# Kernel optimization log

Measured on AMD Instinct MI355X. Metric: run time of the kernel, lower is better.

Reference implementation:

```python
import jax, jax.numpy as jnp
import numpy as np

N = 100000   # nodes
E = 1600000  # edges (avg degree 16)
IN, HID, OUT = 128, 128, 64
EPS = 1e-5


def setup_inputs() -> dict:
    key = jax.random.key(0)
    ks = jax.random.split(key, 8)
    x = jax.random.normal(ks[0], (N, IN), dtype=jnp.float32)
    edge_index = jax.random.randint(ks[1], (2, E), 0, N, dtype=jnp.int64)

    def w(k, i, o):
        return jax.random.normal(k, (i, o), dtype=jnp.float32) / np.float32(np.sqrt(i))

    return {
        'x': x,
        'edge_index': edge_index,
        'W1': w(ks[2], IN, HID), 'b1': jnp.zeros((HID,), jnp.float32),
        'g1': jnp.ones((HID,), jnp.float32), 'be1': jnp.zeros((HID,), jnp.float32),
        'W2': w(ks[3], HID, HID), 'b2': jnp.zeros((HID,), jnp.float32),
        'g2': jnp.ones((HID,), jnp.float32), 'be2': jnp.zeros((HID,), jnp.float32),
        'W3': w(ks[4], HID, OUT), 'b3': jnp.zeros((OUT,), jnp.float32),
    }


def gcn_conv(x, W, b, src, dst, n):
    # GCNConv: x' = D^{-1/2} (A + I) D^{-1/2} X W + b
    h = x @ W                                   # [N, F_out]
    loop = jnp.arange(n, dtype=src.dtype)
    s = jnp.concatenate([src, loop])            # self-loops appended
    d = jnp.concatenate([dst, loop])
    deg = jax.ops.segment_sum(jnp.ones_like(d, dtype=h.dtype), d, num_segments=n)
    dinv = jax.lax.rsqrt(jnp.maximum(deg, 1.0))  # deg >= 1 due to self-loops
    norm = dinv[s] * dinv[d]                     # [E+N]
    out = jax.ops.segment_sum(h[s] * norm[:, None], d, num_segments=n)
    return out + b


def batch_norm(x, gamma, beta):
    m = x.mean(axis=0)
    v = x.var(axis=0)  # biased variance, as used for normalization in torch BN
    return (x - m) * jax.lax.rsqrt(v + EPS) * gamma + beta


def reference(x, edge_index, W1, b1, g1, be1, W2, b2, g2, be2, W3, b3):
    src, dst = edge_index[0], edge_index[1]
    r = x                                        # residual (skip = Identity, in_dim == hidden_dim)
    h = batch_norm(gcn_conv(x, W1, b1, src, dst, N), g1, be1) + r
    r = h
    h = jax.nn.relu(h)                           # dropout p=0 -> identity
    h = batch_norm(gcn_conv(h, W2, b2, src, dst, N), g2, be2) + r
    h = jax.nn.relu(h)
    out = gcn_conv(h, W3, b3, src, dst, N)       # last layer: no bn/skip/relu
    return out
```

## Files before the change

kernel.cpp:

```cpp
#include <hip/hip_runtime.h>

static constexpr int kN = 100000;
static constexpr int kE = 1600000;
static constexpr float kEps = 1e-5f;

static constexpr int kBSH = 9;
static constexpr int kNB = (kN + 511) >> kBSH;
static constexpr int kBCAP = 12288;
static constexpr int kCHUNK = 4096;
static constexpr int kPad = 16;

typedef __attribute__((ext_vector_type(8))) short short8;
typedef __attribute__((ext_vector_type(4))) float float4v;
typedef __attribute__((ext_vector_type(2))) float float2v;

static __device__ inline unsigned short f2bf(float f) {
  union { float f; unsigned int u; } v; v.f = f;
  unsigned int r = v.u + 0x7fffu + ((v.u >> 16) & 1u);
  return (unsigned short)(r >> 16);
}
static __device__ inline float bf2f(unsigned int bits16) {
  union { unsigned int u; float f; } v; v.u = bits16 << 16; return v.f;
}
static __device__ inline unsigned int pack2bf(float lo, float hi) {
  return (unsigned int)f2bf(lo) | ((unsigned int)f2bf(hi) << 16);
}

__global__ __launch_bounds__(512) void bin_k(const int* __restrict__ src,
                                             const int* __restrict__ dst,
                                             int* __restrict__ gcursor,
                                             int2* __restrict__ gstage) {
  __shared__ int s_cnt[256];
  __shared__ int s_scan[256];
  __shared__ int s_base[256];
  __shared__ int s_cur[256];
  __shared__ int s_gb[256];
  __shared__ int2 s_stage[kCHUNK];
  int tid = threadIdx.x;
  int e0 = blockIdx.x * kCHUNK;
  int n = kE - e0; if (n > kCHUNK) n = kCHUNK;
  if (tid < 256) s_cnt[tid] = 0;
  __syncthreads();
  for (int j = tid; j < n; j += 512) {
    atomicAdd(&s_cnt[dst[e0 + j] >> kBSH], 1);
  }
  __syncthreads();
  int v = 0;
  if (tid < 256) { v = s_cnt[tid]; s_scan[tid] = v; }
  __syncthreads();
  #pragma unroll
  for (int o = 1; o < 256; o <<= 1) {
    int t = (tid >= o && tid < 256) ? s_scan[tid - o] : 0;
    __syncthreads();
    if (tid < 256) s_scan[tid] += t;
    __syncthreads();
  }
  if (tid < 256) {
    int excl = s_scan[tid] - v;
    s_base[tid] = excl;
    s_cur[tid] = excl;
  }
  __syncthreads();
  if (tid < kNB && s_cnt[tid] > 0) s_gb[tid] = atomicAdd(&gcursor[tid], s_cnt[tid]);
  for (int j = tid; j < n; j += 512) {
    int s = src[e0 + j];
    int d = dst[e0 + j];
    int p = atomicAdd(&s_cur[d >> kBSH], 1);
    s_stage[p] = make_int2(s, d);
  }
  __syncthreads();
  for (int j = tid; j < n; j += 512) {
    int2 e = s_stage[j];
    int b = e.y >> kBSH;
    gstage[(size_t)b * kBCAP + s_gb[b] + (j - s_base[b])] = e;
  }
}

__global__ __launch_bounds__(256) void alloc_hist_k(const int2* __restrict__ gstage,
                                                    const int* __restrict__ gcursor,
                                                    int* __restrict__ counter,
                                                    int* __restrict__ deg,
                                                    int* __restrict__ row_start,
                                                    float* __restrict__ dinv) {
  __shared__ int s_deg[1 << kBSH];
  __shared__ int s_scan[256];
  __shared__ int s_bcast;
  int b = blockIdx.x, tid = threadIdx.x;
  int n0 = b << kBSH;
  s_deg[tid] = 0;
  s_deg[tid + 256] = 0;
  __syncthreads();
  int cnt = gcursor[b];
  const int2* seg = gstage + (size_t)b * kBCAP;
  for (int j = tid; j < cnt; j += 256) {
    atomicAdd(&s_deg[seg[j].y - n0], 1);
  }
  __syncthreads();
  int i0 = 2 * tid, i1 = 2 * tid + 1;
  int d0 = s_deg[i0], d1 = s_deg[i1];
  int pd0 = (d0 + kPad - 1) & ~(kPad - 1);
  int pd1 = (d1 + kPad - 1) & ~(kPad - 1);
  int sum = pd0 + pd1;
  s_scan[tid] = sum;
  __syncthreads();
  #pragma unroll
  for (int o = 1; o < 256; o <<= 1) {
    int t = (tid >= o) ? s_scan[tid - o] : 0;
    __syncthreads();
    s_scan[tid] += t;
    __syncthreads();
  }
  if (tid == 255) s_bcast = atomicAdd(counter, s_scan[255]);
  __syncthreads();
  int base = s_bcast + s_scan[tid] - sum;
  int node0 = n0 + i0, node1 = n0 + i1;
  if (node0 < kN) {
    deg[node0] = d0;
    row_start[node0] = base;
    dinv[node0] = rsqrtf((float)(d0 + 1));
  }
  if (node1 < kN) {
    deg[node1] = d1;
    row_start[node1] = base + pd0;
    dinv[node1] = rsqrtf((float)(d1 + 1));
  }
}

__global__ __launch_bounds__(256) void scatter2_k(const int2* __restrict__ gstage,
                                                  const int* __restrict__ gcursor,
                                                  const int* __restrict__ rowst,
                                                  const int* __restrict__ deg,
                                                  int* __restrict__ csr_src) {
  __shared__ int s_cur[1 << kBSH];
  int b = blockIdx.x, tid = threadIdx.x;
  int n0 = b << kBSH;
  int nn = kN - n0; if (nn > (1 << kBSH)) nn = 1 << kBSH;
  for (int i = tid; i < nn; i += 256) s_cur[i] = rowst[n0 + i];
  __syncthreads();
  int cnt = gcursor[b];
  const int2* seg = gstage + (size_t)b * kBCAP;
  for (int j = tid; j < cnt; j += 256) {
    int2 e = seg[j];
    int pos = atomicAdd(&s_cur[e.y - n0], 1);
    csr_src[pos] = e.x;
  }
  __syncthreads();
  for (int i = tid; i < nn; i += 256) {
    int d = deg[n0 + i];
    int endp = rowst[n0 + i] + ((d + kPad - 1) & ~(kPad - 1));
    for (int p = s_cur[i]; p < endp; ++p) csr_src[p] = kN;
  }
}

__global__ void convert_w_all_k(const float* __restrict__ W1, const float* __restrict__ W2,
                                const float* __restrict__ W3,
                                unsigned short* __restrict__ wf1,
                                unsigned short* __restrict__ wf2,
                                unsigned short* __restrict__ wf3,
                                unsigned char* __restrict__ hF8,
                                unsigned short* __restrict__ hH) {
  int tid = blockIdx.x * blockDim.x + threadIdx.x;
  const float* W;
  unsigned short* Wf;
  int BNO;
  if (tid < 2048) { W = W1; Wf = wf1; BNO = 128; }
  else if (tid < 4096) { W = W2; Wf = wf2; BNO = 128; tid -= 2048; }
  else if (tid < 5120) { W = W3; Wf = wf3; BNO = 64; tid -= 4096; }
  else if (tid < 5152) {
    ((unsigned int*)(hF8 + (size_t)kN * 128))[tid - 5120] = 0u;
    return;
  } else if (tid < 5184) {
    ((unsigned int*)(hH + (size_t)kN * 64))[tid - 5152] = 0u;
    return;
  } else return;
  int l = tid & 63;
  int frag = tid >> 6;
  int q = frag & 3;
  int t = frag >> 2;
  int n = t * 16 + (l & 15);
  int kbase = q * 32 + ((l >> 4) << 3);
  unsigned short v[8] __attribute__((aligned(16)));
  #pragma unroll
  for (int j = 0; j < 8; ++j) v[j] = f2bf(W[(kbase + j) * BNO + n]);
  ((uint4*)Wf)[tid] = *(const uint4*)v;
}

template <int BNO, bool AF32, bool OUT8>
__global__ __launch_bounds__(256) void gemm_mfma_k(const void* __restrict__ Aptr,
                                                   const unsigned short* __restrict__ Wf,
                                                   const float* __restrict__ dinv,
                                                   void* __restrict__ Cptr,
                                                   float* __restrict__ stats) {
  if (stats && blockIdx.x == 0) stats[threadIdx.x] = 0.f;
  int wid = (int)((blockIdx.x * blockDim.x + threadIdx.x) >> 6);
  if (wid >= kN / 16) return;
  int l = threadIdx.x & 63;
  int r0 = wid * 16;
  short8 a[4];
  if constexpr (AF32) {
    const float* Af = (const float*)Aptr + (size_t)(r0 + (l & 15)) * 128 + ((l >> 4) << 3);
    #pragma unroll
    for (int q = 0; q < 4; ++q) {
      float4 u0 = *(const float4*)(Af + q * 32);
      float4 u1 = *(const float4*)(Af + q * 32 + 4);
      short8 t;
      t[0] = (short)f2bf(u0.x); t[1] = (short)f2bf(u0.y);
      t[2] = (short)f2bf(u0.z); t[3] = (short)f2bf(u0.w);
      t[4] = (short)f2bf(u1.x); t[5] = (short)f2bf(u1.y);
      t[6] = (short)f2bf(u1.z); t[7] = (short)f2bf(u1.w);
      a[q] = t;
    }
  } else {
    const short8* Arow =
        (const short8*)((const unsigned short*)Aptr + (size_t)(r0 + (l & 15)) * 128 + ((l >> 4) << 3));
    #pragma unroll
    for (int q = 0; q < 4; ++q) a[q] = Arow[q * 4];
  }
  const short8* Wv = (const short8*)Wf + l;
  constexpr int NT = BNO / 16;
  float4v acc[NT];
  #pragma unroll
  for (int t = 0; t < NT; ++t) {
    acc[t] = (float4v){0.f, 0.f, 0.f, 0.f};
    #pragma unroll
    for (int q = 0; q < 4; ++q) {
      short8 b = Wv[(t * 4 + q) * 64];
      acc[t] = __builtin_amdgcn_mfma_f32_16x16x32_bf16(a[q], b, acc[t], 0, 0, 0);
    }
  }
  int orow = r0 + ((l >> 4) << 2);
  int ocol = l & 15;
  float dv[4];
  #pragma unroll
  for (int r = 0; r < 4; ++r) dv[r] = dinv[orow + r];
  #pragma unroll
  for (int t = 0; t < NT; ++t) {
    #pragma unroll
    for (int r = 0; r < 4; ++r) {
      float val = acc[t][r] * dv[r];
      if constexpr (OUT8) {
        unsigned int u = __builtin_amdgcn_cvt_pk_fp8_f32(val, val, 0u, false);
        ((unsigned char*)Cptr)[(size_t)(orow + r) * BNO + t * 16 + ocol] = (unsigned char)(u & 0xffu);
      } else {
        ((unsigned short*)Cptr)[(size_t)(orow + r) * BNO + t * 16 + ocol] = f2bf(val);
      }
    }
  }
}

__global__ __launch_bounds__(256) void aggregate128_k(
    const unsigned char* __restrict__ H8, const int* __restrict__ row_start,
    const int* __restrict__ deg, const int* __restrict__ csr_src,
    const float* __restrict__ dinv, const float* __restrict__ bias,
    unsigned int* __restrict__ outp, float* __restrict__ stats) {
  __shared__ float s_sum[128], s_sq[128];
  int tid = threadIdx.x;
  if (tid < 128) { s_sum[tid] = 0.f; s_sq[tid] = 0.f; }
  __syncthreads();
  int lane = tid & 63;
  int qt = lane >> 4;
  int ql = lane & 15;
  int nwaves = gridDim.x * (blockDim.x >> 6);
  int gwave = (int)((blockIdx.x * blockDim.x + tid) >> 6);
  const uint2* H2 = (const uint2*)H8;
  float4 blo = ((const float4*)bias)[2 * ql];
  float4 bhi = ((const float4*)bias)[2 * ql + 1];
  float st[8] = {0.f, 0.f, 0.f, 0.f, 0.f, 0.f, 0.f, 0.f};
  float sqa[8] = {0.f, 0.f, 0.f, 0.f, 0.f, 0.f, 0.f, 0.f};
  auto accum = [](float (&a)[8], uint2 v) {
    float2v p0 = __builtin_amdgcn_cvt_pk_f32_fp8(v.x, false);
    float2v p1 = __builtin_amdgcn_cvt_pk_f32_fp8(v.x, true);
    float2v p2 = __builtin_amdgcn_cvt_pk_f32_fp8(v.y, false);
    float2v p3 = __builtin_amdgcn_cvt_pk_f32_fp8(v.y, true);
    a[0] += p0.x; a[1] += p0.y; a[2] += p1.x; a[3] += p1.y;
    a[4] += p2.x; a[5] += p2.y; a[6] += p3.x; a[7] += p3.y;
  };
  int node = gwave;
  int rs = 0, pd = 0;
  float di = 1.f;
  int ec = kN;
  if (node < kN) {
    rs = row_start[node];
    pd = (deg[node] + kPad - 1) & ~(kPad - 1);
    di = dinv[node];
    ec = csr_src[rs + lane];
  }
  while (node < kN) {
    int cur_rs = rs, cur_pd = pd, cur_e = ec;
    float cur_di = di;
    int nxt = node + nwaves;
    if (nxt < kN) {
      rs = row_start[nxt];
      pd = (deg[nxt] + kPad - 1) & ~(kPad - 1);
      di = dinv[nxt];
      ec = csr_src[rs + lane];
    }
    float a[8] = {0.f, 0.f, 0.f, 0.f, 0.f, 0.f, 0.f, 0.f};
    uint2 vself = H2[(size_t)node * 16 + ql];
    int nb = cur_pd >> 4;
    int nb4 = nb > 4 ? 4 : nb;
    for (int i = 0; i < nb4; ++i) {
      int s[4];
      uint2 v[4];
      #pragma unroll
      for (int j = 0; j < 4; ++j) s[j] = __shfl(cur_e, i * 16 + 4 * j + qt, 64);
      #pragma unroll
      for (int j = 0; j < 4; ++j) v[j] = H2[(size_t)s[j] * 16 + ql];
      #pragma unroll
      for (int j = 0; j < 4; ++j) accum(a, v[j]);
    }
    for (int i = 4; i < nb; ++i) {
      int ee = csr_src[cur_rs + i * 16 + (lane & 15)];
      int s[4];
      uint2 v[4];
      #pragma unroll
      for (int j = 0; j < 4; ++j) s[j] = __shfl(ee, 4 * j + qt, 64);
      #pragma unroll
      for (int j = 0; j < 4; ++j) v[j] = H2[(size_t)s[j] * 16 + ql];
      #pragma unroll
      for (int j = 0; j < 4; ++j) accum(a, v[j]);
    }
    #pragma unroll
    for (int j = 0; j < 8; ++j) {
      a[j] += __shfl_xor(a[j], 16, 64);
      a[j] += __shfl_xor(a[j], 32, 64);
    }
    accum(a, vself);
    float o[8];
    o[0] = cur_di * a[0] + blo.x; o[1] = cur_di * a[1] + blo.y;
    o[2] = cur_di * a[2] + blo.z; o[3] = cur_di * a[3] + blo.w;
    o[4] = cur_di * a[4] + bhi.x; o[5] = cur_di * a[5] + bhi.y;
    o[6] = cur_di * a[6] + bhi.z; o[7] = cur_di * a[7] + bhi.w;
    if (qt == 0) {
      uint4 ov;
      ov.x = pack2bf(o[0], o[1]); ov.y = pack2bf(o[2], o[3]);
      ov.z = pack2bf(o[4], o[5]); ov.w = pack2bf(o[6], o[7]);
      ((uint4*)outp)[(size_t)node * 16 + ql] = ov;
      #pragma unroll
      for (int j = 0; j < 8; ++j) { st[j] += o[j]; sqa[j] += o[j] * o[j]; }
    }
    node = nxt;
  }
  if (qt == 0) {
    #pragma unroll
    for (int j = 0; j < 8; ++j) {
      atomicAdd(&s_sum[8 * ql + j], st[j]);
      atomicAdd(&s_sq[8 * ql + j], sqa[j]);
    }
  }
  __syncthreads();
  if (tid < 128) {
    atomicAdd(&stats[tid], s_sum[tid]);
    atomicAdd(&stats[128 + tid], s_sq[tid]);
  }
}

__global__ __launch_bounds__(256) void aggregate64_k(
    const unsigned short* __restrict__ Hb, const int* __restrict__ row_start,
    const int* __restrict__ deg, const int* __restrict__ csr_src,
    const float* __restrict__ dinv, const float* __restrict__ bias,
    float* __restrict__ outp) {
  int tid = threadIdx.x;
  int lane = tid & 63;
  int qt = lane >> 4;
  int ql = lane & 15;
  int nwaves = gridDim.x * (blockDim.x >> 6);
  int gwave = (int)((blockIdx.x * blockDim.x + tid) >> 6);
  const uint2* H2 = (const uint2*)Hb;
  float4 b4 = ((const float4*)bias)[ql];
  auto accum = [](float (&a)[4], uint2 v) {
    a[0] += bf2f(v.x & 0xffffu); a[1] += bf2f(v.x >> 16);
    a[2] += bf2f(v.y & 0xffffu); a[3] += bf2f(v.y >> 16);
  };
  int node = gwave;
  int rs = 0, pd = 0;
  float di = 1.f;
  int ec = kN;
  if (node < kN) {
    rs = row_start[node];
    pd = (deg[node] + kPad - 1) & ~(kPad - 1);
    di = dinv[node];
    ec = csr_src[rs + lane];
  }
  while (node < kN) {
    int cur_rs = rs, cur_pd = pd, cur_e = ec;
    float cur_di = di;
    int nxt = node + nwaves;
    if (nxt < kN) {
      rs = row_start[nxt];
      pd = (deg[nxt] + kPad - 1) & ~(kPad - 1);
      di = dinv[nxt];
      ec = csr_src[rs + lane];
    }
    float a[4] = {0.f, 0.f, 0.f, 0.f};
    uint2 vself = H2[(size_t)node * 16 + ql];
    int nb = cur_pd >> 4;
    int nb4 = nb > 4 ? 4 : nb;
    for (int i = 0; i < nb4; ++i) {
      int s[4];
      uint2 v[4];
      #pragma unroll
      for (int j = 0; j < 4; ++j) s[j] = __shfl(cur_e, i * 16 + 4 * j + qt, 64);
      #pragma unroll
      for (int j = 0; j < 4; ++j) v[j] = H2[(size_t)s[j] * 16 + ql];
      #pragma unroll
      for (int j = 0; j < 4; ++j) accum(a, v[j]);
    }
    for (int i = 4; i < nb; ++i) {
      int ee = csr_src[cur_rs + i * 16 + (lane & 15)];
      int s[4];
      uint2 v[4];
      #pragma unroll
      for (int j = 0; j < 4; ++j) s[j] = __shfl(ee, 4 * j + qt, 64);
      #pragma unroll
      for (int j = 0; j < 4; ++j) v[j] = H2[(size_t)s[j] * 16 + ql];
      #pragma unroll
      for (int j = 0; j < 4; ++j) accum(a, v[j]);
    }
    #pragma unroll
    for (int j = 0; j < 4; ++j) {
      a[j] += __shfl_xor(a[j], 16, 64);
      a[j] += __shfl_xor(a[j], 32, 64);
    }
    accum(a, vself);
    if (qt == 0) {
      ((float4*)outp)[(size_t)node * 16 + ql] =
          make_float4(cur_di * a[0] + b4.x, cur_di * a[1] + b4.y,
                      cur_di * a[2] + b4.z, cur_di * a[3] + b4.w);
    }
    node = nxt;
  }
}

template <bool WRITE_Z, bool RF32>
__global__ void bn_apply_res_k(const unsigned int* __restrict__ a, const void* __restrict__ rp,
                               const float* __restrict__ stats, const float* __restrict__ g,
                               const float* __restrict__ be, unsigned int* __restrict__ z,
                               unsigned int* __restrict__ rb) {
  __shared__ float lss[256];
  int t = threadIdx.x;
  if (t < 128) {
    float mean = stats[t] * (1.f / kN);
    float var = stats[128 + t] * (1.f / kN) - mean * mean;
    float inv = rsqrtf(var + kEps);
    float sc = g[t] * inv;
    lss[t] = sc;
    lss[128 + t] = be[t] - mean * sc;
  }
  __syncthreads();
  int idx = blockIdx.x * blockDim.x + t;
  if (idx >= kN * 16) return;
  uint4 av = ((const uint4*)a)[idx];
  float r[8];
  if constexpr (RF32) {
    float4 r0 = ((const float4*)rp)[idx * 2];
    float4 r1 = ((const float4*)rp)[idx * 2 + 1];
    r[0] = r0.x; r[1] = r0.y; r[2] = r0.z; r[3] = r0.w;
    r[4] = r1.x; r[5] = r1.y; r[6] = r1.z; r[7] = r1.w;
  } else {
    uint4 rv = ((const uint4*)rp)[idx];
    r[0] = bf2f(rv.x & 0xffffu); r[1] = bf2f(rv.x >> 16);
    r[2] = bf2f(rv.y & 0xffffu); r[3] = bf2f(rv.y >> 16);
    r[4] = bf2f(rv.z & 0xffffu); r[5] = bf2f(rv.z >> 16);
    r[6] = bf2f(rv.w & 0xffffu); r[7] = bf2f(rv.w >> 16);
  }
  int c = (idx & 15) * 8;
  float o[8];
  unsigned int apk[4] = {av.x, av.y, av.z, av.w};
  #pragma unroll
  for (int j = 0; j < 4; ++j) {
    o[2 * j]     = lss[c + 2 * j] * bf2f(apk[j] & 0xffffu) + lss[128 + c + 2 * j] + r[2 * j];
    o[2 * j + 1] = lss[c + 2 * j + 1] * bf2f(apk[j] >> 16) + lss[128 + c + 2 * j + 1] + r[2 * j + 1];
  }
  if (WRITE_Z) {
    uint4 zv;
    zv.x = pack2bf(o[0], o[1]); zv.y = pack2bf(o[2], o[3]);
    zv.z = pack2bf(o[4], o[5]); zv.w = pack2bf(o[6], o[7]);
    ((uint4*)z)[idx] = zv;
  }
  uint4 hv;
  hv.x = pack2bf(fmaxf(o[0], 0.f), fmaxf(o[1], 0.f));
  hv.y = pack2bf(fmaxf(o[2], 0.f), fmaxf(o[3], 0.f));
  hv.z = pack2bf(fmaxf(o[4], 0.f), fmaxf(o[5], 0.f));
  hv.w = pack2bf(fmaxf(o[6], 0.f), fmaxf(o[7], 0.f));
  ((uint4*)rb)[idx] = hv;
}

extern "C" void kernel_launch(void* const* d_in, const int* in_sizes, int n_in,
                              void* d_out, int out_size, void* d_ws, size_t ws_size,
                              hipStream_t stream) {
  const float* x   = (const float*)d_in[0];
  const int*   ei  = (const int*)d_in[1];
  const float* W1  = (const float*)d_in[2];
  const float* b1  = (const float*)d_in[3];
  const float* g1  = (const float*)d_in[4];
  const float* be1 = (const float*)d_in[5];
  const float* W2  = (const float*)d_in[6];
  const float* b2  = (const float*)d_in[7];
  const float* g2  = (const float*)d_in[8];
  const float* be2 = (const float*)d_in[9];
  const float* W3  = (const float*)d_in[10];
  const float* b3  = (const float*)d_in[11];
  float* outp = (float*)d_out;

  const int* src = ei;
  const int* dst = ei + kE;

  char* ws = (char*)d_ws;
  size_t off = 0;
  auto alloc = [&](size_t bytes) -> void* {
    void* p = ws + off;
    off = (off + bytes + 255) & ~size_t(255);
    return p;
  };
  unsigned char* hF8 = (unsigned char*)alloc((size_t)(kN + 1) * 128);
  unsigned short* hH = (unsigned short*)alloc((size_t)(kN + 1) * 64 * 2);
  unsigned int* aB = (unsigned int*)alloc((size_t)kN * 64 * 4);
  unsigned int* zC = (unsigned int*)alloc((size_t)kN * 64 * 4);
  unsigned int* hb = (unsigned int*)alloc((size_t)kN * 64 * 4);
  int*   csr_src  = (int*)alloc((size_t)(3200000 + 64) * 4);
  int2*  gstage   = (int2*)alloc((size_t)kNB * kBCAP * 8);
  int*   gcursor  = (int*)alloc((kNB + 1) * 4);
  int*   counter  = gcursor + kNB;
  int*   deg      = (int*)alloc((size_t)kN * 4);
  float* dinv     = (float*)alloc((size_t)kN * 4);
  int*   rowst    = (int*)alloc((size_t)kN * 4);
  float* stats    = (float*)alloc(256 * 4);
  unsigned short* wf1 = (unsigned short*)alloc(128 * 128 * 2);
  unsigned short* wf2 = (unsigned short*)alloc(128 * 128 * 2);
  unsigned short* wf3 = (unsigned short*)alloc(128 * 64 * 2);

  const int TB = 256;
  int blkBin = (kE + kCHUNK - 1) / kCHUNK;
  int blkGemm = (kN / 16 + 3) / 4;
  int blkApply = kN * 16 / TB;
  const int blkAgg = 2048;

  hipMemsetAsync(gcursor, 0, (kNB + 1) * 4, stream);
  bin_k<<<blkBin, 512, 0, stream>>>(src, dst, gcursor, gstage);
  alloc_hist_k<<<kNB, TB, 0, stream>>>(gstage, gcursor, counter, deg, rowst, dinv);
  scatter2_k<<<kNB, TB, 0, stream>>>(gstage, gcursor, rowst, deg, csr_src);
  convert_w_all_k<<<21, TB, 0, stream>>>(W1, W2, W3, wf1, wf2, wf3, hF8, hH);

  gemm_mfma_k<128, true, true><<<blkGemm, 256, 0, stream>>>(x, wf1, dinv, hF8, stats);
  aggregate128_k<<<blkAgg, TB, 0, stream>>>(hF8, rowst, deg, csr_src, dinv, b1, aB, stats);
  bn_apply_res_k<true, true><<<blkApply, TB, 0, stream>>>(aB, x, stats, g1, be1, zC, hb);

  gemm_mfma_k<128, false, true><<<blkGemm, 256, 0, stream>>>((const unsigned short*)hb, wf2, dinv, hF8, stats);
  aggregate128_k<<<blkAgg, TB, 0, stream>>>(hF8, rowst, deg, csr_src, dinv, b2, aB, stats);
  bn_apply_res_k<false, false><<<blkApply, TB, 0, stream>>>(aB, zC, stats, g2, be2, nullptr, hb);

  gemm_mfma_k<64, false, false><<<blkGemm, 256, 0, stream>>>((const unsigned short*)hb, wf3, dinv, hH, nullptr);
  aggregate64_k<<<blkAgg, TB, 0, stream>>>(hH, rowst, deg, csr_src, dinv, b3, outp);
}
```

Baseline: 423.8 us.

## Fuse batch-norm apply and residual into next GEMM prologue, add nontemporal loads

Removes the separate bn_apply_res kernels and folds BN scale/shift, residual add, ReLU and bf16 packing into the A-operand load of the following MFMA GEMM. This drops the intermediate hb buffer round trip and two launches. The stats buffer is split into two halves zeroed up front in the weight-conversion kernel, so the GEMM no longer resets stats. The aggregation kernels also switch CSR/index loads and output stores to nontemporal, which may help or hurt cache reuse of metadata.

```diff
diff --git a/kernel.cpp b/kernel.cpp
--- a/kernel.cpp
+++ b/kernel.cpp
@@ -13,6 +13,7 @@
 typedef __attribute__((ext_vector_type(8))) short short8;
 typedef __attribute__((ext_vector_type(4))) float float4v;
 typedef __attribute__((ext_vector_type(2))) float float2v;
+typedef __attribute__((ext_vector_type(4))) unsigned int uint4v;
 
 static __device__ inline unsigned short f2bf(float f) {
   union { float f; unsigned int u; } v; v.f = f;
@@ -158,7 +159,8 @@
                                 unsigned short* __restrict__ wf2,
                                 unsigned short* __restrict__ wf3,
                                 unsigned char* __restrict__ hF8,
-                                unsigned short* __restrict__ hH) {
+                                unsigned short* __restrict__ hH,
+                                float* __restrict__ stats) {
   int tid = blockIdx.x * blockDim.x + threadIdx.x;
   const float* W;
   unsigned short* Wf;
@@ -172,6 +174,9 @@
   } else if (tid < 5184) {
     ((unsigned int*)(hH + (size_t)kN * 64))[tid - 5152] = 0u;
     return;
+  } else if (tid < 5696) {
+    stats[tid - 5184] = 0.f;
+    return;
   } else return;
   int l = tid & 63;
   int frag = tid >> 6;
@@ -185,19 +190,35 @@
   ((uint4*)Wf)[tid] = *(const uint4*)v;
 }
 
-template <int BNO, bool AF32, bool OUT8>
+template <int BNO, int AMODE, bool OUT8>
 __global__ __launch_bounds__(256) void gemm_mfma_k(const void* __restrict__ Aptr,
+                                                   const void* __restrict__ Rptr,
+                                                   const float* __restrict__ stats,
+                                                   const float* __restrict__ g,
+                                                   const float* __restrict__ be,
+                                                   unsigned int* __restrict__ Zptr,
                                                    const unsigned short* __restrict__ Wf,
                                                    const float* __restrict__ dinv,
-                                                   void* __restrict__ Cptr,
-                                                   float* __restrict__ stats) {
-  if (stats && blockIdx.x == 0) stats[threadIdx.x] = 0.f;
+                                                   void* __restrict__ Cptr) {
+  __shared__ float lss[256];
+  if constexpr (AMODE != 0) {
+    int t = threadIdx.x;
+    if (t < 128) {
+      float mean = stats[t] * (1.f / kN);
+      float var = stats[128 + t] * (1.f / kN) - mean * mean;
+      float inv = rsqrtf(var + kEps);
+      float sc = g[t] * inv;
+      lss[t] = sc;
+      lss[128 + t] = be[t] - mean * sc;
+    }
+    __syncthreads();
+  }
   int wid = (int)((blockIdx.x * blockDim.x + threadIdx.x) >> 6);
   if (wid >= kN / 16) return;
   int l = threadIdx.x & 63;
   int r0 = wid * 16;
   short8 a[4];
-  if constexpr (AF32) {
+  if constexpr (AMODE == 0) {
     const float* Af = (const float*)Aptr + (size_t)(r0 + (l & 15)) * 128 + ((l >> 4) << 3);
     #pragma unroll
     for (int q = 0; q < 4; ++q) {
@@ -211,10 +232,45 @@
       a[q] = t;
     }
   } else {
-    const short8* Arow =
-        (const short8*)((const unsigned short*)Aptr + (size_t)(r0 + (l & 15)) * 128 + ((l >> 4) << 3));
-    #pragma unroll
-    for (int q = 0; q < 4; ++q) a[q] = Arow[q * 4];
+    int row = r0 + (l & 15);
+    int cg0 = l >> 4;
+    const uint4* Ab = (const uint4*)Aptr + (size_t)row * 16;
+    #pragma unroll
+    for (int q = 0; q < 4; ++q) {
+      int cg = q * 4 + cg0;
+      int c0 = cg * 8;
+      uint4 av = Ab[cg];
+      float r[8];
+      if constexpr (AMODE == 1) {
+        const float4* Rf = (const float4*)Rptr + (size_t)row * 32 + cg * 2;
+        float4 r0v = Rf[0], r1v = Rf[1];
+        r[0] = r0v.x; r[1] = r0v.y; r[2] = r0v.z; r[3] = r0v.w;
+        r[4] = r1v.x; r[5] = r1v.y; r[6] = r1v.z; r[7] = r1v.w;
+      } else {
+        uint4 rv = ((const uint4*)Rptr)[(size_t)row * 16 + cg];
+        r[0] = bf2f(rv.x & 0xffffu); r[1] = bf2f(rv.x >> 16);
+        r[2] = bf2f(rv.y & 0xffffu); r[3] = bf2f(rv.y >> 16);
+        r[4] = bf2f(rv.z & 0xffffu); r[5] = bf2f(rv.z >> 16);
+        r[6] = bf2f(rv.w & 0xffffu); r[7] = bf2f(rv.w >> 16);
+      }
+      unsigned int apk[4] = {av.x, av.y, av.z, av.w};
+      float o[8];
+      #pragma unroll
+      for (int j = 0; j < 4; ++j) {
+        o[2 * j]     = lss[c0 + 2 * j] * bf2f(apk[j] & 0xffffu) + lss[128 + c0 + 2 * j] + r[2 * j];
+        o[2 * j + 1] = lss[c0 + 2 * j + 1] * bf2f(apk[j] >> 16) + lss[128 + c0 + 2 * j + 1] + r[2 * j + 1];
+      }
+      if constexpr (AMODE == 1) {
+        uint4 zv;
+        zv.x = pack2bf(o[0], o[1]); zv.y = pack2bf(o[2], o[3]);
+        zv.z = pack2bf(o[4], o[5]); zv.w = pack2bf(o[6], o[7]);
+        ((uint4*)Zptr)[(size_t)row * 16 + cg] = zv;
+      }
+      short8 t;
+      #pragma unroll
+      for (int j = 0; j < 8; ++j) t[j] = (short)f2bf(fmaxf(o[j], 0.f));
+      a[q] = t;
+    }
   }
   const short8* Wv = (const short8*)Wf + l;
   constexpr int NT = BNO / 16;
@@ -280,20 +336,20 @@
   float di = 1.f;
   int ec = kN;
   if (node < kN) {
-    rs = row_start[node];
-    pd = (deg[node] + kPad - 1) & ~(kPad - 1);
-    di = dinv[node];
-    ec = csr_src[rs + lane];
+    rs = __builtin_nontemporal_load(row_start + node);
+    pd = (__builtin_nontemporal_load(deg + node) + kPad - 1) & ~(kPad - 1);
+    di = __builtin_nontemporal_load(dinv + node);
+    ec = __builtin_nontemporal_load(csr_src + rs + lane);
   }
   while (node < kN) {
     int cur_rs = rs, cur_pd = pd, cur_e = ec;
     float cur_di = di;
     int nxt = node + nwaves;
     if (nxt < kN) {
-      rs = row_start[nxt];
-      pd = (deg[nxt] + kPad - 1) & ~(kPad - 1);
-      di = dinv[nxt];
-      ec = csr_src[rs + lane];
+      rs = __builtin_nontemporal_load(row_start + nxt);
+      pd = (__builtin_nontemporal_load(deg + nxt) + kPad - 1) & ~(kPad - 1);
+      di = __builtin_nontemporal_load(dinv + nxt);
+      ec = __builtin_nontemporal_load(csr_src + rs + lane);
     }
     float a[8] = {0.f, 0.f, 0.f, 0.f, 0.f, 0.f, 0.f, 0.f};
     uint2 vself = H2[(size_t)node * 16 + ql];
@@ -310,7 +366,7 @@
       for (int j = 0; j < 4; ++j) accum(a, v[j]);
     }
     for (int i = 4; i < nb; ++i) {
-      int ee = csr_src[cur_rs + i * 16 + (lane & 15)];
+      int ee = __builtin_nontemporal_load(csr_src + cur_rs + i * 16 + (lane & 15));
       int s[4];
       uint2 v[4];
       #pragma unroll
@@ -332,10 +388,10 @@
     o[4] = cur_di * a[4] + bhi.x; o[5] = cur_di * a[5] + bhi.y;
     o[6] = cur_di * a[6] + bhi.z; o[7] = cur_di * a[7] + bhi.w;
     if (qt == 0) {
-      uint4 ov;
-      ov.x = pack2bf(o[0], o[1]); ov.y = pack2bf(o[2], o[3]);
-      ov.z = pack2bf(o[4], o[5]); ov.w = pack2bf(o[6], o[7]);
-      ((uint4*)outp)[(size_t)node * 16 + ql] = ov;
+      uint4v ov;
+      ov[0] = pack2bf(o[0], o[1]); ov[1] = pack2bf(o[2], o[3]);
+      ov[2] = pack2bf(o[4], o[5]); ov[3] = pack2bf(o[6], o[7]);
+      __builtin_nontemporal_store(ov, (uint4v*)outp + (size_t)node * 16 + ql);
       #pragma unroll
       for (int j = 0; j < 8; ++j) { st[j] += o[j]; sqa[j] += o[j] * o[j]; }
     }
@@ -377,20 +433,20 @@
   float di = 1.f;
   int ec = kN;
   if (node < kN) {
-    rs = row_start[node];
-    pd = (deg[node] + kPad - 1) & ~(kPad - 1);
-    di = dinv[node];
-    ec = csr_src[rs + lane];
+    rs = __builtin_nontemporal_load(row_start + node);
+    pd = (__builtin_nontemporal_load(deg + node) + kPad - 1) & ~(kPad - 1);
+    di = __builtin_nontemporal_load(dinv + node);
+    ec = __builtin_nontemporal_load(csr_src + rs + lane);
   }
   while (node < kN) {
     int cur_rs = rs, cur_pd = pd, cur_e = ec;
     float cur_di = di;
     int nxt = node + nwaves;
     if (nxt < kN) {
-      rs = row_start[nxt];
-      pd = (deg[nxt] + kPad - 1) & ~(kPad - 1);
-      di = dinv[nxt];
-      ec = csr_src[rs + lane];
+      rs = __builtin_nontemporal_load(row_start + nxt);
+      pd = (__builtin_nontemporal_load(deg + nxt) + kPad - 1) & ~(kPad - 1);
+      di = __builtin_nontemporal_load(dinv + nxt);
+      ec = __builtin_nontemporal_load(csr_src + rs + lane);
     }
     float a[4] = {0.f, 0.f, 0.f, 0.f};
     uint2 vself = H2[(size_t)node * 16 + ql];
@@ -407,7 +463,7 @@
       for (int j = 0; j < 4; ++j) accum(a, v[j]);
     }
     for (int i = 4; i < nb; ++i) {
-      int ee = csr_src[cur_rs + i * 16 + (lane & 15)];
+      int ee = __builtin_nontemporal_load(csr_src + cur_rs + i * 16 + (lane & 15));
       int s[4];
       uint2 v[4];
       #pragma unroll
@@ -424,66 +480,13 @@
     }
     accum(a, vself);
     if (qt == 0) {
-      ((float4*)outp)[(size_t)node * 16 + ql] =
-          make_float4(cur_di * a[0] + b4.x, cur_di * a[1] + b4.y,
-                      cur_di * a[2] + b4.z, cur_di * a[3] + b4.w);
+      float4v ov;
+      ov[0] = cur_di * a[0] + b4.x; ov[1] = cur_di * a[1] + b4.y;
+      ov[2] = cur_di * a[2] + b4.z; ov[3] = cur_di * a[3] + b4.w;
+      __builtin_nontemporal_store(ov, (float4v*)outp + (size_t)node * 16 + ql);
     }
     node = nxt;
   }
-}
-
-template <bool WRITE_Z, bool RF32>
-__global__ void bn_apply_res_k(const unsigned int* __restrict__ a, const void* __restrict__ rp,
-                               const float* __restrict__ stats, const float* __restrict__ g,
-                               const float* __restrict__ be, unsigned int* __restrict__ z,
-                               unsigned int* __restrict__ rb) {
-  __shared__ float lss[256];
-  int t = threadIdx.x;
-  if (t < 128) {
-    float mean = stats[t] * (1.f / kN);
-    float var = stats[128 + t] * (1.f / kN) - mean * mean;
-    float inv = rsqrtf(var + kEps);
-    float sc = g[t] * inv;
-    lss[t] = sc;
-    lss[128 + t] = be[t] - mean * sc;
-  }
-  __syncthreads();
-  int idx = blockIdx.x * blockDim.x + t;
-  if (idx >= kN * 16) return;
-  uint4 av = ((const uint4*)a)[idx];
-  float r[8];
-  if constexpr (RF32) {
-    float4 r0 = ((const float4*)rp)[idx * 2];
-    float4 r1 = ((const float4*)rp)[idx * 2 + 1];
-    r[0] = r0.x; r[1] = r0.y; r[2] = r0.z; r[3] = r0.w;
-    r[4] = r1.x; r[5] = r1.y; r[6] = r1.z; r[7] = r1.w;
-  } else {
-    uint4 rv = ((const uint4*)rp)[idx];
-    r[0] = bf2f(rv.x & 0xffffu); r[1] = bf2f(rv.x >> 16);
-    r[2] = bf2f(rv.y & 0xffffu); r[3] = bf2f(rv.y >> 16);
-    r[4] = bf2f(rv.z & 0xffffu); r[5] = bf2f(rv.z >> 16);
-    r[6] = bf2f(rv.w & 0xffffu); r[7] = bf2f(rv.w >> 16);
-  }
-  int c = (idx & 15) * 8;
-  float o[8];
-  unsigned int apk[4] = {av.x, av.y, av.z, av.w};
-  #pragma unroll
-  for (int j = 0; j < 4; ++j) {
-    o[2 * j]     = lss[c + 2 * j] * bf2f(apk[j] & 0xffffu) + lss[128 + c + 2 * j] + r[2 * j];
-    o[2 * j + 1] = lss[c + 2 * j + 1] * bf2f(apk[j] >> 16) + lss[128 + c + 2 * j + 1] + r[2 * j + 1];
-  }
-  if (WRITE_Z) {
-    uint4 zv;
-    zv.x = pack2bf(o[0], o[1]); zv.y = pack2bf(o[2], o[3]);
-    zv.z = pack2bf(o[4], o[5]); zv.w = pack2bf(o[6], o[7]);
-    ((uint4*)z)[idx] = zv;
-  }
-  uint4 hv;
-  hv.x = pack2bf(fmaxf(o[0], 0.f), fmaxf(o[1], 0.f));
-  hv.y = pack2bf(fmaxf(o[2], 0.f), fmaxf(o[3], 0.f));
-  hv.z = pack2bf(fmaxf(o[4], 0.f), fmaxf(o[5], 0.f));
-  hv.w = pack2bf(fmaxf(o[6], 0.f), fmaxf(o[7], 0.f));
-  ((uint4*)rb)[idx] = hv;
 }
 
 extern "C" void kernel_launch(void* const* d_in, const int* in_sizes, int n_in,
@@ -517,7 +520,6 @@
   unsigned short* hH = (unsigned short*)alloc((size_t)(kN + 1) * 64 * 2);
   unsigned int* aB = (unsigned int*)alloc((size_t)kN * 64 * 4);
   unsigned int* zC = (unsigned int*)alloc((size_t)kN * 64 * 4);
-  unsigned int* hb = (unsigned int*)alloc((size_t)kN * 64 * 4);
   int*   csr_src  = (int*)alloc((size_t)(3200000 + 64) * 4);
   int2*  gstage   = (int2*)alloc((size_t)kNB * kBCAP * 8);
   int*   gcursor  = (int*)alloc((kNB + 1) * 4);
@@ -525,7 +527,9 @@
   int*   deg      = (int*)alloc((size_t)kN * 4);
   float* dinv     = (float*)alloc((size_t)kN * 4);
   int*   rowst    = (int*)alloc((size_t)kN * 4);
-  float* stats    = (float*)alloc(256 * 4);
+  float* stats    = (float*)alloc(512 * 4);
+  float* statsA   = stats;
+  float* statsB   = stats + 256;
   unsigned short* wf1 = (unsigned short*)alloc(128 * 128 * 2);
   unsigned short* wf2 = (unsigned short*)alloc(128 * 128 * 2);
   unsigned short* wf3 = (unsigned short*)alloc(128 * 64 * 2);
@@ -533,23 +537,23 @@
   const int TB = 256;
   int blkBin = (kE + kCHUNK - 1) / kCHUNK;
   int blkGemm = (kN / 16 + 3) / 4;
-  int blkApply = kN * 16 / TB;
   const int blkAgg = 2048;
 
   hipMemsetAsync(gcursor, 0, (kNB + 1) * 4, stream);
   bin_k<<<blkBin, 512, 0, stream>>>(src, dst, gcursor, gstage);
   alloc_hist_k<<<kNB, TB, 0, stream>>>(gstage, gcursor, counter, deg, rowst, dinv);
   scatter2_k<<<kNB, TB, 0, stream>>>(gstage, gcursor, rowst, deg, csr_src);
-  convert_w_all_k<<<21, TB, 0, stream>>>(W1, W2, W3, wf1, wf2, wf3, hF8, hH);
-
-  gemm_mfma_k<128, true, true><<<blkGemm, 256, 0, stream>>>(x, wf1, dinv, hF8, stats);
-  aggregate128_k<<<blkAgg, TB, 0, stream>>>(hF8, rowst, deg, csr_src, dinv, b1, aB, stats);
-  bn_apply_res_k<true, true><<<blkApply, TB, 0, stream>>>(aB, x, stats, g1, be1, zC, hb);
-
-  gemm_mfma_k<128, false, true><<<blkGemm, 256, 0, stream>>>((const unsigned short*)hb, wf2, dinv, hF8, stats);
-  aggregate128_k<<<blkAgg, TB, 0, stream>>>(hF8, rowst, deg, csr_src, dinv, b2, aB, stats);
-  bn_apply_res_k<false, false><<<blkApply, TB, 0, stream>>>(aB, zC, stats, g2, be2, nullptr, hb);
-
-  gemm_mfma_k<64, false, false><<<blkGemm, 256, 0, stream>>>((const unsigned short*)hb, wf3, dinv, hH, nullptr);
+  convert_w_all_k<<<23, TB, 0, stream>>>(W1, W2, W3, wf1, wf2, wf3, hF8, hH, stats);
+
+  gemm_mfma_k<128, 0, true><<<blkGemm, TB, 0, stream>>>(
+      x, nullptr, nullptr, nullptr, nullptr, nullptr, wf1, dinv, hF8);
+  aggregate128_k<<<blkAgg, TB, 0, stream>>>(hF8, rowst, deg, csr_src, dinv, b1, aB, statsA);
+
+  gemm_mfma_k<128, 1, true><<<blkGemm, TB, 0, stream>>>(
+      aB, x, statsA, g1, be1, zC, wf2, dinv, hF8);
+  aggregate128_k<<<blkAgg, TB, 0, stream>>>(hF8, rowst, deg, csr_src, dinv, b2, aB, statsB);
+
+  gemm_mfma_k<64, 2, false><<<blkGemm, TB, 0, stream>>>(
+      aB, zC, statsB, g2, be2, nullptr, wf3, dinv, hH);
   aggregate64_k<<<blkAgg, TB, 0, stream>>>(hH, rowst, deg, csr_src, dinv, b3, outp);
 }
```

Result: slower. 453.0 us (+6.9%).
